# Kernel tuning notes

Hardware: AMD Instinct MI355X
Metric: run time of the kernel (lower is better)

Reference implementation:

```python
import jax, jax.numpy as jnp
import numpy as np

B, D_IN, D_OUT, N_CACHE = 2048, 1024, 512, 50000


def setup_inputs() -> dict:
    key = jax.random.key(0)
    k1, k2, k3, k4, k5 = jax.random.split(key, 5)
    scale = 1.0 / np.sqrt(D_IN)
    return {
        "x": jax.random.normal(k1, (B, D_IN), dtype=jnp.float32),
        "W": jax.random.normal(k2, (D_OUT, D_IN), dtype=jnp.float32) * scale,
        "b": jax.random.normal(k3, (D_OUT,), dtype=jnp.float32) * 0.01,
        "cache_image_features": jax.random.normal(k4, (N_CACHE, D_OUT), dtype=jnp.float32),
        "cache_text_features": jax.random.normal(k5, (N_CACHE, D_OUT), dtype=jnp.float32),
        "beta": jnp.ones((1,), dtype=jnp.float32),
        "alpha": jnp.ones((1,), dtype=jnp.float32),
    }


def reference(x, W, b, cache_image_features, cache_text_features, beta, alpha):
    # projected_x = x @ W.T + b  -> [B, D_OUT]
    projected_x = jnp.einsum('bi,oi->bo', x, W) + b
    # similarity over cached image features -> [B, N_CACHE]
    similarity = jnp.einsum('bo,no->bn', projected_x, cache_image_features)
    weights = jax.nn.softmax(beta * similarity, axis=-1)
    # retrieve from cached text features -> [B, D_OUT]
    retrieved = jnp.einsum('bn,no->bo', weights, cache_text_features)
    return projected_x + alpha * retrieved
```

## Files before the change

### kernel.cpp

```cpp
#include <hip/hip_runtime.h>
#include <hip/hip_bf16.h>
#include <math.h>

typedef _Float16 f16;
typedef __attribute__((ext_vector_type(8))) _Float16 f16x8;
typedef __attribute__((ext_vector_type(4))) float f32x4;
typedef __attribute__((ext_vector_type(16))) float f32x16;
typedef __attribute__((ext_vector_type(4))) unsigned int u32x4;
typedef __attribute__((ext_vector_type(2))) unsigned int u32x2;

#define MFMA16(A, B, C) __builtin_amdgcn_mfma_f32_16x16x32_f16(A, B, C, 0, 0, 0)
#define MFMA32(A, B, C) __builtin_amdgcn_mfma_f32_32x32x16_f16(A, B, C, 0, 0, 0)
#define AS1 __attribute__((address_space(1)))
#define AS3 __attribute__((address_space(3)))

__device__ __forceinline__ void gld16(const char* g, char* l) {
  __builtin_amdgcn_global_load_lds((const AS1 void*)g, (AS3 void*)l, 16, 0, 0);
}

__device__ __forceinline__ unsigned pk2(float a, float b) {
  auto h = __builtin_amdgcn_cvt_pkrtz(a, b);
  return __builtin_bit_cast(unsigned, h);
}

namespace {
constexpr int kB = 2048;
constexpr int kNch = 16, kChunk = 3125, kNit = 98;
constexpr int kKRows = 50176;
constexpr int kVStride = 3200;
constexpr size_t WS_PROJ = 0;
constexpr size_t WS_QHI  = WS_PROJ + (size_t)2048 * 512 * 4;
constexpr size_t WS_M    = WS_QHI + (size_t)2048 * 512 * 2;
constexpr size_t WS_L    = WS_M + (size_t)kNch * kB * 4;
constexpr size_t WS_PV   = WS_L + (size_t)kNch * kB * 4;
constexpr size_t WS_K16  = WS_PV + (size_t)kNch * kB * 512 * 2;
constexpr size_t WS_VT   = WS_K16 + (size_t)kKRows * 512 * 2;
constexpr int LDS_K0 = 0, LDS_K1 = 33280;
constexpr int LDS_V0 = 66560, LDS_V1 = 99328;
constexpr int LDS_S  = 132096;
constexpr int LDS_P  = 148480;
constexpr int LDS_FAC = 156672;
constexpr int LDS_FLG = 157184;
constexpr int LDS_SZ  = 157696;
}

__global__ __launch_bounds__(256) void convk_kernel(const float* __restrict__ src,
                                                    f16* __restrict__ dst) {
  const size_t e = ((size_t)blockIdx.x * 256 + threadIdx.x) * 8;
  const int row = (int)(e >> 9);
  float4 a = make_float4(0.f, 0.f, 0.f, 0.f), b = a;
  if (row < 50000) {
    a = *(const float4*)(src + e);
    b = *(const float4*)(src + e + 4);
  }
  f16x8 h;
  h[0] = (f16)a.x; h[1] = (f16)a.y; h[2] = (f16)a.z; h[3] = (f16)a.w;
  h[4] = (f16)b.x; h[5] = (f16)b.y; h[6] = (f16)b.z; h[7] = (f16)b.w;
  *(f16x8*)(dst + e) = h;
}

__global__ __launch_bounds__(256) void transv_kernel(const float* __restrict__ Vf,
                                                     f16* __restrict__ Vt) {
  __shared__ float tile[64][65];
  const int kt = blockIdx.x, colt = blockIdx.y, ch = blockIdx.z;
  const int t = threadIdx.x;
  const int kbase = kt * 64, col0 = colt * 64;
  {
    const int key = t >> 2, cseg = (t & 3) * 16;
    const int kk = kbase + key;
    float4 v0 = make_float4(0.f, 0.f, 0.f, 0.f), v1 = v0, v2 = v0, v3 = v0;
    if (kk < kChunk) {
      const float* s = Vf + (size_t)(ch * kChunk + kk) * 512 + col0 + cseg;
      v0 = *(const float4*)(s);
      v1 = *(const float4*)(s + 4);
      v2 = *(const float4*)(s + 8);
      v3 = *(const float4*)(s + 12);
    }
    float* tr = &tile[key][cseg];
    tr[0] = v0.x;  tr[1] = v0.y;  tr[2] = v0.z;  tr[3] = v0.w;
    tr[4] = v1.x;  tr[5] = v1.y;  tr[6] = v1.z;  tr[7] = v1.w;
    tr[8] = v2.x;  tr[9] = v2.y;  tr[10] = v2.z; tr[11] = v2.w;
    tr[12] = v3.x; tr[13] = v3.y; tr[14] = v3.z; tr[15] = v3.w;
  }
  __syncthreads();
  {
    const int col = t >> 2, kw = (t & 3) * 16;
    f16x8 h0, h1;
    #pragma unroll
    for (int u = 0; u < 8; u++) h0[u] = (f16)tile[kw + u][col];
    #pragma unroll
    for (int u = 0; u < 8; u++) h1[u] = (f16)tile[kw + 8 + u][col];
    f16* d = Vt + ((size_t)ch * 512 + col0 + col) * kVStride + kbase + kw;
    *(f16x8*)(d) = h0;
    *(f16x8*)(d + 8) = h1;
  }
}

__global__ __launch_bounds__(256) void gemm1_kernel(
    const float* __restrict__ x, const float* __restrict__ W,
    const float* __restrict__ bias, const float* __restrict__ beta_p,
    float* __restrict__ proj, f16* __restrict__ qhi)
{
  __shared__ f16 xh[2][64][40], xl[2][64][40], wh[2][64][40], wl[2][64][40];
  const int t = threadIdx.x;
  const int lane = t & 63, w = t >> 6;
  const int wr = w >> 1, wc = w & 1;
  const int g = lane >> 4, j = lane & 15;
  const int m0 = blockIdx.x * 64, n0 = blockIdx.y * 64;
  const int srow = t >> 2;
  const int soff = (t & 3) * 8;
  const float bscale = beta_p[0] * 1.44269504f;

  const f32x4 fzero = {0.f, 0.f, 0.f, 0.f};
  f32x4 acc[2][2], acc2[2][2];
  #pragma unroll
  for (int a = 0; a < 2; a++)
    #pragma unroll
    for (int bb = 0; bb < 2; bb++) { acc[a][bb] = fzero; acc2[a][bb] = fzero; }

  auto stage = [&](int k0s, int buf) {
    const float* xs  = x + (size_t)(m0 + srow) * 1024 + k0s + soff;
    const float* wsr = W + (size_t)(n0 + srow) * 1024 + k0s + soff;
    f16x8 hx, lx, hw, lw;
    #pragma unroll
    for (int i = 0; i < 8; i++) {
      float v = xs[i];
      f16 h = (f16)v;
      hx[i] = h;
      lx[i] = (f16)((v - (float)h) * 2048.0f);
      float u = wsr[i];
      f16 hu = (f16)u;
      hw[i] = hu;
      lw[i] = (f16)((u - (float)hu) * 2048.0f);
    }
    *(f16x8*)&xh[buf][srow][soff] = hx;
    *(f16x8*)&xl[buf][srow][soff] = lx;
    *(f16x8*)&wh[buf][srow][soff] = hw;
    *(f16x8*)&wl[buf][srow][soff] = lw;
  };

  stage(0, 0);
  for (int ks = 0; ks < 32; ks++) {
    __syncthreads();
    if (ks < 31) stage((ks + 1) * 32, (ks + 1) & 1);
    const int buf = ks & 1;
    f16x8 ah[2], al[2], bh[2], bl[2];
    #pragma unroll
    for (int mf = 0; mf < 2; mf++) {
      const int r = wr * 32 + mf * 16 + j;
      ah[mf] = *(const f16x8*)&xh[buf][r][g * 8];
      al[mf] = *(const f16x8*)&xl[buf][r][g * 8];
      const int cc = wc * 32 + mf * 16 + j;
      bh[mf] = *(const f16x8*)&wh[buf][cc][g * 8];
      bl[mf] = *(const f16x8*)&wl[buf][cc][g * 8];
    }
    #pragma unroll
    for (int mf = 0; mf < 2; mf++)
      #pragma unroll
      for (int nf = 0; nf < 2; nf++) {
        acc[mf][nf]  = MFMA16(ah[mf], bh[nf], acc[mf][nf]);
        acc2[mf][nf] = MFMA16(ah[mf], bl[nf], acc2[mf][nf]);
        acc2[mf][nf] = MFMA16(al[mf], bh[nf], acc2[mf][nf]);
      }
  }

  #pragma unroll
  for (int mf = 0; mf < 2; mf++)
    #pragma unroll
    for (int nf = 0; nf < 2; nf++)
      #pragma unroll
      for (int r = 0; r < 4; r++) {
        const int m = m0 + wr * 32 + mf * 16 + g * 4 + r;
        const int n = n0 + wc * 32 + nf * 16 + j;
        float p = acc[mf][nf][r] + acc2[mf][nf][r] * (1.0f / 2048.0f) + bias[n];
        proj[(size_t)m * 512 + n] = p;
        qhi[(size_t)m * 512 + n] = (f16)(p * bscale);
      }
}

__global__ __launch_bounds__(512, 2) void attn_kernel(
    const f16* __restrict__ K16, const f16* __restrict__ Vt16,
    const f16* __restrict__ qhi_ws,
    float* __restrict__ m_part, float* __restrict__ l_part,
    f16* __restrict__ pvn)
{
  extern __shared__ char smem[];
  const int t = threadIdx.x, lane = t & 63, w = t >> 6;
  const int c = lane & 31, h = lane >> 5;
  const int qb = w & 3, dh = w >> 2;
  const int qp = w & 1, cq = w >> 1;
  const int ch = blockIdx.x & 15, qt = blockIdx.x >> 4;
  const int q0 = qt * 128;

  char* const Kb0 = smem + LDS_K0;
  char* const Kb1 = smem + LDS_K1;
  char* const Vb0 = smem + LDS_V0;
  char* const Vb1 = smem + LDS_V1;
  char* const Sq  = smem + LDS_S + qb * 4096;
  char* const Pq  = smem + LDS_P + qb * 2048;
  float* const facl = (float*)(smem + LDS_FAC);
  int* const flg = (int*)(smem + LDS_FLG);

  f16x8 Qf[16];
  {
    const f16* qsrc = qhi_ws + (size_t)(q0 + qb * 32 + c) * 512 + dh * 256 + h * 8;
    #pragma unroll
    for (int i = 0; i < 16; i++) Qf[i] = *(const f16x8*)(qsrc + i * 16);
  }
  __builtin_amdgcn_sched_barrier(0);

  const char* const Kg = (const char*)K16 + (size_t)(ch * kChunk) * 1024;
  const char* const Vg = (const char*)Vt16 + (size_t)ch * 512 * (kVStride * 2);
  const int vlo = (((lane & 3) ^ ((lane >> 3) & 3)) << 4);

  auto stageK = [&](int it2, char* dstbuf) {
    const char* src = Kg + (size_t)(it2 * 32 + w * 4) * 1024 + lane * 16;
    char* dst = dstbuf + (w * 4) * 1040 + lane * 16;
    #pragma unroll
    for (int u = 0; u < 4; u++) gld16(src + u * 1024, dst + u * 1040);
  };
  auto stageV = [&](int it2, char* dstbuf) {
    const char* src = Vg + (size_t)(w * 64 + (lane >> 2)) * (kVStride * 2) + it2 * 64 + vlo;
    char* dst = dstbuf + (w * 4) * 1024 + lane * 16;
    #pragma unroll
    for (int u = 0; u < 4; u++)
      gld16(src + (size_t)(u * 16) * (kVStride * 2), dst + u * 1024);
  };

  const int kroff = c * 1040 + dh * 512 + h * 16;
  const int vbase = (cq * 128 + c) * 64;
  const int vswz = ((c >> 1) & 3) << 4;
  const int voff0 = (0 + h * 16) ^ vswz;
  const int voff1 = (32 + h * 16) ^ vswz;
  const char* const slotA = smem + LDS_P + (2 * qp) * 2048 + lane * 16;
  const char* const slotB = smem + LDS_P + (2 * qp + 1) * 2048 + lane * 16;

  f32x16 O[2][4];
  #pragma unroll
  for (int ql = 0; ql < 2; ql++)
    #pragma unroll
    for (int cb = 0; cb < 4; cb++)
      #pragma unroll
      for (int r = 0; r < 16; r++) O[ql][cb][r] = 0.f;
  float mrow = -INFINITY, lrow = 0.f;

  auto pvstep = [&](const char* Vp) {
    const int f0 = flg[2 * qp];
    const int f1 = flg[2 * qp + 1];
    const f16x8 pb00 = *(const f16x8*)(slotA);
    const f16x8 pb01 = *(const f16x8*)(slotA + 1024);
    const f16x8 pb10 = *(const f16x8*)(slotB);
    const f16x8 pb11 = *(const f16x8*)(slotB + 1024);
    if (f0) {
      const float fc0 = facl[(2 * qp) * 32 + c];
      #pragma unroll
      for (int cb = 0; cb < 4; cb++)
        #pragma unroll
        for (int r = 0; r < 16; r++) O[0][cb][r] *= fc0;
    }
    if (f1) {
      const float fc1 = facl[(2 * qp + 1) * 32 + c];
      #pragma unroll
      for (int cb = 0; cb < 4; cb++)
        #pragma unroll
        for (int r = 0; r < 16; r++) O[1][cb][r] *= fc1;
    }
    __builtin_amdgcn_s_setprio(1);
    #pragma unroll
    for (int cb = 0; cb < 4; cb++) {
      f16x8 a0 = *(const f16x8*)(Vp + cb * 2048 + voff0);
      f16x8 a1 = *(const f16x8*)(Vp + cb * 2048 + voff1);
      O[0][cb] = MFMA32(a0, pb00, O[0][cb]);
      O[0][cb] = MFMA32(a1, pb01, O[0][cb]);
      O[1][cb] = MFMA32(a0, pb10, O[1][cb]);
      O[1][cb] = MFMA32(a1, pb11, O[1][cb]);
    }
    __builtin_amdgcn_s_setprio(0);
  };

  stageK(0, Kb0);
  stageV(0, Vb0);
  asm volatile("s_waitcnt vmcnt(4)" ::: "memory");
  __builtin_amdgcn_s_barrier();

  for (int it = 0; it < kNit; it++) {
    const int p = it & 1;
    const char* const Kp = (p ? Kb1 : Kb0) + kroff;

    if (it + 1 < kNit) stageK(it + 1, p ? Kb0 : Kb1);

    f32x16 S;
    #pragma unroll
    for (int r = 0; r < 16; r++) S[r] = 0.f;
    __builtin_amdgcn_s_setprio(1);
    #pragma unroll
    for (int i = 0; i < 16; i++) {
      f16x8 a = *(const f16x8*)(Kp + i * 32);
      S = MFMA32(a, Qf[i], S);
    }
    __builtin_amdgcn_s_setprio(0);

    if (dh == 1) {
      f32x4 v0 = {S[0], S[1], S[2], S[3]};
      f32x4 v1 = {S[4], S[5], S[6], S[7]};
      f32x4 v2 = {S[8], S[9], S[10], S[11]};
      f32x4 v3 = {S[12], S[13], S[14], S[15]};
      *(f32x4*)(Sq + 0 * 1024 + lane * 16) = v0;
      *(f32x4*)(Sq + 1 * 1024 + lane * 16) = v1;
      *(f32x4*)(Sq + 2 * 1024 + lane * 16) = v2;
      *(f32x4*)(Sq + 3 * 1024 + lane * 16) = v3;
    }

    if (it > 0) pvstep((p ? Vb0 : Vb1) + vbase);

    asm volatile("s_waitcnt lgkmcnt(0)" ::: "memory");
    __builtin_amdgcn_s_barrier();

    if (it + 1 < kNit) stageV(it + 1, p ? Vb0 : Vb1);

    if (dh == 0) {
      #pragma unroll
      for (int cc = 0; cc < 4; cc++) {
        f32x4 v = *(const f32x4*)(Sq + cc * 1024 + lane * 16);
        S[4 * cc + 0] += v.x; S[4 * cc + 1] += v.y;
        S[4 * cc + 2] += v.z; S[4 * cc + 3] += v.w;
      }
      if (it == kNit - 1) {
        #pragma unroll
        for (int r = 0; r < 16; r++) {
          const int key = it * 32 + (r & 3) + 8 * (r >> 2) + 4 * h;
          if (key >= kChunk) S[r] = -INFINITY;
        }
      }
      float pm = S[0];
      #pragma unroll
      for (int r = 1; r < 16; r++) pm = fmaxf(pm, S[r]);
      pm = fmaxf(pm, __shfl_xor(pm, 32));
      const int need = __any(pm > mrow + 11.5416f);
      float fc = 1.0f;
      if (need) {
        const float mn = fmaxf(mrow, pm);
        fc = exp2f(mrow - mn);
        mrow = mn;
      }
      float pr[16], rs = 0.f;
      #pragma unroll
      for (int r = 0; r < 16; r++) { pr[r] = exp2f(S[r] - mrow); rs += pr[r]; }
      rs += __shfl_xor(rs, 32);
      lrow = lrow * fc + rs;
      unsigned pA0 = pk2(pr[0], pr[1]),  pA1 = pk2(pr[2], pr[3]);
      unsigned pB0 = pk2(pr[4], pr[5]),  pB1 = pk2(pr[6], pr[7]);
      unsigned pC0 = pk2(pr[8], pr[9]),  pC1 = pk2(pr[10], pr[11]);
      unsigned pD0 = pk2(pr[12], pr[13]), pD1 = pk2(pr[14], pr[15]);
      unsigned sA0 = __shfl_xor(pA0, 32), sA1 = __shfl_xor(pA1, 32);
      unsigned sB0 = __shfl_xor(pB0, 32), sB1 = __shfl_xor(pB1, 32);
      unsigned sC0 = __shfl_xor(pC0, 32), sC1 = __shfl_xor(pC1, 32);
      unsigned sD0 = __shfl_xor(pD0, 32), sD1 = __shfl_xor(pD1, 32);
      u32x4 B0, B1;
      B0[0] = h ? sB0 : pA0;  B0[1] = h ? sB1 : pA1;
      B0[2] = h ? pB0 : sA0;  B0[3] = h ? pB1 : sA1;
      B1[0] = h ? sD0 : pC0;  B1[1] = h ? sD1 : pC1;
      B1[2] = h ? pD0 : sC0;  B1[3] = h ? pD1 : sC1;
      *(u32x4*)(Pq + lane * 16) = B0;
      *(u32x4*)(Pq + 1024 + lane * 16) = B1;
      if (need && h == 0) facl[qb * 32 + c] = fc;
      if (lane == 0) flg[qb] = need;
    }
    if (it + 1 < kNit)
      asm volatile("s_waitcnt lgkmcnt(0) vmcnt(4)" ::: "memory");
    else
      asm volatile("s_waitcnt lgkmcnt(0) vmcnt(0)" ::: "memory");
    __builtin_amdgcn_s_barrier();
  }

  pvstep((((kNit - 1) & 1) ? Vb1 : Vb0) + vbase);

  __builtin_amdgcn_s_barrier();
  if (dh == 0) {
    const float iv = 1.0f / lrow;
    if (lane < 32) {
      m_part[ch * kB + q0 + qb * 32 + c] = mrow;
      l_part[ch * kB + q0 + qb * 32 + c] = lrow;
      facl[qb * 32 + c] = iv;
    }
  }
  asm volatile("s_waitcnt lgkmcnt(0)" ::: "memory");
  __builtin_amdgcn_s_barrier();
  const float iv0 = facl[(2 * qp) * 32 + c];
  const float iv1 = facl[(2 * qp + 1) * 32 + c];

  const size_t pvb = ((size_t)ch * kB + q0) * 512;
  #pragma unroll
  for (int ql = 0; ql < 2; ql++) {
    const int qrow = (2 * qp + ql) * 32 + c;
    const float iv = ql ? iv1 : iv0;
    #pragma unroll
    for (int cb = 0; cb < 4; cb++) {
      const int C = cq * 128 + cb * 32;
      #pragma unroll
      for (int a = 0; a < 4; a++) {
        unsigned lo = pk2(O[ql][cb][4 * a + 0] * iv, O[ql][cb][4 * a + 1] * iv);
        unsigned hi = pk2(O[ql][cb][4 * a + 2] * iv, O[ql][cb][4 * a + 3] * iv);
        u32x2 v = {lo, hi};
        *(u32x2*)(pvn + pvb + (size_t)qrow * 512 + C + 8 * a + 4 * h) = v;
      }
    }
  }
}

__global__ __launch_bounds__(256) void combine_kernel(
    const float* __restrict__ proj, const float* __restrict__ m_part,
    const float* __restrict__ l_part, const f16* __restrict__ pvn,
    const float* __restrict__ alpha_p, float* __restrict__ out)
{
  const int row = blockIdx.x;
  const int t = threadIdx.x;
  const float alpha = alpha_p[0];
  float M = -INFINITY;
  #pragma unroll
  for (int c = 0; c < kNch; c++) M = fmaxf(M, m_part[c * kB + row]);
  float gl[kNch];
  float T = 0.f;
  #pragma unroll
  for (int c = 0; c < kNch; c++) {
    gl[c] = exp2f(m_part[c * kB + row] - M) * l_part[c * kB + row];
    T += gl[c];
  }
  const float s = alpha / T;
  #pragma unroll
  for (int half = 0; half < 2; half++) {
    const int col = t + half * 256;
    float acc = 0.f;
    #pragma unroll
    for (int c = 0; c < kNch; c++)
      acc += gl[c] * (float)pvn[((size_t)c * kB + row) * 512 + col];
    out[(size_t)row * 512 + col] = proj[(size_t)row * 512 + col] + acc * s;
  }
}

extern "C" void kernel_launch(void* const* d_in, const int* in_sizes, int n_in,
                              void* d_out, int out_size, void* d_ws, size_t ws_size,
                              hipStream_t stream) {
  (void)in_sizes; (void)n_in; (void)out_size; (void)ws_size;
  const float* x     = (const float*)d_in[0];
  const float* W     = (const float*)d_in[1];
  const float* bias  = (const float*)d_in[2];
  const float* cimg  = (const float*)d_in[3];
  const float* ctxt  = (const float*)d_in[4];
  const float* beta  = (const float*)d_in[5];
  const float* alpha = (const float*)d_in[6];
  float* out = (float*)d_out;
  char* ws = (char*)d_ws;

  float* proj = (float*)(ws + WS_PROJ);
  f16*   qhi  = (f16*)(ws + WS_QHI);
  float* mp   = (float*)(ws + WS_M);
  float* lp   = (float*)(ws + WS_L);
  f16*   pvn  = (f16*)(ws + WS_PV);
  f16*   K16  = (f16*)(ws + WS_K16);
  f16*   Vt16 = (f16*)(ws + WS_VT);

  (void)hipFuncSetAttribute((const void*)attn_kernel,
                            hipFuncAttributeMaxDynamicSharedMemorySize, LDS_SZ);

  convk_kernel<<<(kKRows * 512 / 8 + 255) / 256, 256, 0, stream>>>(cimg, K16);
  transv_kernel<<<dim3(kVStride / 64, 8, kNch), 256, 0, stream>>>(ctxt, Vt16);
  gemm1_kernel<<<dim3(32, 8), 256, 0, stream>>>(x, W, bias, beta, proj, qhi);
  attn_kernel<<<256, 512, LDS_SZ, stream>>>(K16, Vt16, qhi, mp, lp, pvn);
  combine_kernel<<<2048, 256, 0, stream>>>(proj, mp, lp, pvn, alpha, out);
}
```

Before: 382.0 us.

## Reschedule PV step around barrier and tree-reduce softmax max and sum

Splits the PV step into a P-fragment load plus rescale, issued early, and an MFMA part that now runs after the S-exchange barrier, overlapping the softmax computation. The V-stage prefetch moves after a new extra barrier at the end of each iteration. It also replaces the serial max and sum chains in the softmax with tree reductions to shorten dependency chains. The added barrier per iteration and the delayed V prefetch may reduce load/compute overlap.

```diff
diff --git a/kernel.cpp b/kernel.cpp
--- a/kernel.cpp
+++ b/kernel.cpp
@@ -244,13 +244,14 @@
       for (int r = 0; r < 16; r++) O[ql][cb][r] = 0.f;
   float mrow = -INFINITY, lrow = 0.f;
 
-  auto pvstep = [&](const char* Vp) {
+  f16x8 pb00, pb01, pb10, pb11;
+  auto pvload = [&]() {
     const int f0 = flg[2 * qp];
     const int f1 = flg[2 * qp + 1];
-    const f16x8 pb00 = *(const f16x8*)(slotA);
-    const f16x8 pb01 = *(const f16x8*)(slotA + 1024);
-    const f16x8 pb10 = *(const f16x8*)(slotB);
-    const f16x8 pb11 = *(const f16x8*)(slotB + 1024);
+    pb00 = *(const f16x8*)(slotA);
+    pb01 = *(const f16x8*)(slotA + 1024);
+    pb10 = *(const f16x8*)(slotB);
+    pb11 = *(const f16x8*)(slotB + 1024);
     if (f0) {
       const float fc0 = facl[(2 * qp) * 32 + c];
       #pragma unroll
@@ -265,6 +266,8 @@
         #pragma unroll
         for (int r = 0; r < 16; r++) O[1][cb][r] *= fc1;
     }
+  };
+  auto pvmfma = [&](const char* Vp) {
     __builtin_amdgcn_s_setprio(1);
     #pragma unroll
     for (int cb = 0; cb < 4; cb++) {
@@ -288,6 +291,7 @@
     const char* const Kp = (p ? Kb1 : Kb0) + kroff;
 
     if (it + 1 < kNit) stageK(it + 1, p ? Kb0 : Kb1);
+    if (it > 0) pvload();
 
     f32x16 S;
     #pragma unroll
@@ -310,13 +314,10 @@
       *(f32x4*)(Sq + 2 * 1024 + lane * 16) = v2;
       *(f32x4*)(Sq + 3 * 1024 + lane * 16) = v3;
     }
-
-    if (it > 0) pvstep((p ? Vb0 : Vb1) + vbase);
-
     asm volatile("s_waitcnt lgkmcnt(0)" ::: "memory");
     __builtin_amdgcn_s_barrier();
 
-    if (it + 1 < kNit) stageV(it + 1, p ? Vb0 : Vb1);
+    if (it > 0) pvmfma((p ? Vb0 : Vb1) + vbase);
 
     if (dh == 0) {
       #pragma unroll
@@ -332,9 +333,14 @@
           if (key >= kChunk) S[r] = -INFINITY;
         }
       }
-      float pm = S[0];
-      #pragma unroll
-      for (int r = 1; r < 16; r++) pm = fmaxf(pm, S[r]);
+      float t0 = fmaxf(S[0], S[1]),  t1 = fmaxf(S[2], S[3]);
+      float t2 = fmaxf(S[4], S[5]),  t3 = fmaxf(S[6], S[7]);
+      float t4 = fmaxf(S[8], S[9]),  t5 = fmaxf(S[10], S[11]);
+      float t6 = fmaxf(S[12], S[13]), t7 = fmaxf(S[14], S[15]);
+      t0 = fmaxf(t0, t1); t2 = fmaxf(t2, t3);
+      t4 = fmaxf(t4, t5); t6 = fmaxf(t6, t7);
+      t0 = fmaxf(t0, t2); t4 = fmaxf(t4, t6);
+      float pm = fmaxf(t0, t4);
       pm = fmaxf(pm, __shfl_xor(pm, 32));
       const int need = __any(pm > mrow + 11.5416f);
       float fc = 1.0f;
@@ -343,9 +349,14 @@
         fc = exp2f(mrow - mn);
         mrow = mn;
       }
-      float pr[16], rs = 0.f;
-      #pragma unroll
-      for (int r = 0; r < 16; r++) { pr[r] = exp2f(S[r] - mrow); rs += pr[r]; }
+      float pr[16];
+      #pragma unroll
+      for (int r = 0; r < 16; r++) pr[r] = exp2f(S[r] - mrow);
+      float s0 = (pr[0] + pr[1]) + (pr[2] + pr[3]);
+      float s1 = (pr[4] + pr[5]) + (pr[6] + pr[7]);
+      float s2 = (pr[8] + pr[9]) + (pr[10] + pr[11]);
+      float s3 = (pr[12] + pr[13]) + (pr[14] + pr[15]);
+      float rs = (s0 + s1) + (s2 + s3);
       rs += __shfl_xor(rs, 32);
       lrow = lrow * fc + rs;
       unsigned pA0 = pk2(pr[0], pr[1]),  pA1 = pk2(pr[2], pr[3]);
@@ -366,15 +377,22 @@
       if (need && h == 0) facl[qb * 32 + c] = fc;
       if (lane == 0) flg[qb] = need;
     }
-    if (it + 1 < kNit)
-      asm volatile("s_waitcnt lgkmcnt(0) vmcnt(4)" ::: "memory");
-    else
-      asm volatile("s_waitcnt lgkmcnt(0) vmcnt(0)" ::: "memory");
+    asm volatile("s_waitcnt lgkmcnt(0)" ::: "memory");
     __builtin_amdgcn_s_barrier();
-  }
-
-  pvstep((((kNit - 1) & 1) ? Vb1 : Vb0) + vbase);
-
+
+    if (it + 1 < kNit) {
+      stageV(it + 1, p ? Vb0 : Vb1);
+      asm volatile("s_waitcnt vmcnt(4)" ::: "memory");
+    } else {
+      asm volatile("s_waitcnt vmcnt(0)" ::: "memory");
+    }
+    __builtin_amdgcn_s_barrier();
+  }
+
+  pvload();
+  pvmfma((((kNit - 1) & 1) ? Vb1 : Vb0) + vbase);
+
+  asm volatile("s_waitcnt lgkmcnt(0)" ::: "memory");
   __builtin_amdgcn_s_barrier();
   if (dh == 0) {
     const float iv = 1.0f / lrow;
```

Result: slower. 401.8 us (+5.2%).
